# Kernel tuning notes

Measured on AMD Instinct MI355X. Metric: run time of the kernel, lower is better.

The kernel has to match this reference:

```python
import jax, jax.numpy as jnp
import numpy as np

N_NODES = 50000
N_EDGES = 800000
D_FEAT = 64


def setup_inputs() -> dict:
    key = jax.random.key(0)
    k_x, k_e, k_w = jax.random.split(key, 3)
    x = jax.random.normal(k_x, (N_NODES, D_FEAT), dtype=jnp.float32)
    edge_index = jax.random.randint(k_e, (2, N_EDGES), 0, N_NODES, dtype=jnp.int64)
    # message MLP params (phi_Theta): single linear + ReLU
    W = jax.random.normal(k_w, (D_FEAT, D_FEAT), dtype=jnp.float32) / np.sqrt(D_FEAT)
    b = jnp.zeros((D_FEAT,), dtype=jnp.float32)
    return {"x": x, "edge_index": edge_index, "W": W, "b": b}


def reference(x, edge_index, W, b):
    # flow = source_to_target: messages flow from edge_index[0] (j) to edge_index[1] (i)
    src = edge_index[0]  # j: source nodes (gather)
    dst = edge_index[1]  # i: target nodes (scatter index)
    n_nodes = x.shape[0]
    # __collect__: index_select gather of source node features -> x_j [E, D]
    x_j = x[src]
    # message: per-edge MLP  phi(x_j) = relu(x_j W + b)
    msg = jax.nn.relu(jnp.einsum('ed,df->ef', x_j, W) + b)
    # aggregate: scatter-add into target nodes (aggr='add', dim_size = size_i)
    out = jax.ops.segment_sum(msg, dst, num_segments=n_nodes)
    # update: identity
    return out
```

## Files before the change

kernel.cpp:

```cpp
#include <hip/hip_runtime.h>
#include <hip/hip_bf16.h>

#define D 64
#define CAP 32
#define OVF_CAP 16384
#define NSHARD 8

__device__ __forceinline__ float bf2f(unsigned short u) {
    return __uint_as_float((unsigned int)u << 16);
}
__device__ __forceinline__ unsigned short f2bf(float f) {
    unsigned int u = __float_as_uint(f);
    unsigned int r = (u + 0x7fffu + ((u >> 16) & 1u)) >> 16;
    return (unsigned short)r;
}

__global__ __launch_bounds__(256) void node_mlp_kernel(
    const float* __restrict__ x, const float* __restrict__ W,
    const float* __restrict__ b, unsigned short* __restrict__ m,
    int* __restrict__ cnt, int* __restrict__ ovf_cnt, int n_nodes) {
    for (int i = blockIdx.x * blockDim.x + threadIdx.x; i < n_nodes;
         i += gridDim.x * blockDim.x) cnt[i] = 0;
    if (blockIdx.x == 0 && threadIdx.x == 0) *ovf_cnt = 0;

    const int lane = threadIdx.x & 63;
    float w[D];
    #pragma unroll
    for (int k = 0; k < D; ++k) w[k] = W[k * D + lane];
    const float bias = b[lane];

    const int wave = (blockIdx.x * blockDim.x + threadIdx.x) >> 6;
    const int nwaves = (gridDim.x * blockDim.x) >> 6;

    for (int row = wave; row < n_nodes; row += nwaves) {
        const float4* xr = (const float4*)(x + (size_t)row * D);
        float acc = bias;
        #pragma unroll
        for (int kk = 0; kk < D / 4; ++kk) {
            float4 xv = xr[kk];
            acc = fmaf(xv.x, w[4 * kk + 0], acc);
            acc = fmaf(xv.y, w[4 * kk + 1], acc);
            acc = fmaf(xv.z, w[4 * kk + 2], acc);
            acc = fmaf(xv.w, w[4 * kk + 3], acc);
        }
        m[(size_t)row * D + lane] = f2bf(fmaxf(acc, 0.0f));
    }
}

__global__ __launch_bounds__(256) void append_kernel(
    const int* __restrict__ src, const int* __restrict__ dst,
    int* __restrict__ cnt, unsigned short* __restrict__ slots,
    int* __restrict__ ovf_cnt, unsigned int* __restrict__ ovf,
    int n_edges, int blocks_per_shard) {
    const int shard = blockIdx.x & (NSHARD - 1);
    const int p = blockIdx.x >> 3;
    const int chunk = (n_edges + blocks_per_shard - 1) / blocks_per_shard;
    const int beg = p * chunk;
    const int end = min(beg + chunk, n_edges);

    for (int e = beg + (int)threadIdx.x; e < end; e += 256) {
        int d = dst[e];
        if ((d & (NSHARD - 1)) != shard) continue;
        int s = src[e];
        int pos = atomicAdd(&cnt[d], 1);
        if (pos < CAP) {
            slots[(size_t)d * CAP + pos] = (unsigned short)s;
        } else {
            int op = atomicAdd(ovf_cnt, 1);
            if (op < OVF_CAP)
                ovf[op] = ((unsigned int)d << 16) | (unsigned int)s;
        }
    }
}

__global__ __launch_bounds__(256) void gather_kernel(
    const unsigned short* __restrict__ slots, const int* __restrict__ cnt,
    const unsigned short* __restrict__ m,
    const int* __restrict__ ovf_cnt, const unsigned int* __restrict__ ovf,
    float* __restrict__ out, int n_nodes) {
    const int grp = blockIdx.x >> 3;
    const int xcd = blockIdx.x & 7;
    int node = grp * 32 + ((threadIdx.x >> 6) << 3) + xcd;
    if (node >= n_nodes) return;
    node = __builtin_amdgcn_readfirstlane(node);

    const int lane = threadIdx.x & 63;

    const int c = cnt[node];
    const int cc = min(c, CAP);
    const unsigned int* __restrict__ row =
        (const unsigned int*)(slots + (size_t)node * CAP);

    float acc = 0.0f;
    int k = 0;
    for (; k + 16 <= cc; k += 16) {
        unsigned int p[8];
        #pragma unroll
        for (int i = 0; i < 8; ++i) p[i] = row[(k >> 1) + i];
        float v[16];
        #pragma unroll
        for (int i = 0; i < 8; ++i) {
            const unsigned short* ba = m + (size_t)(p[i] & 0xFFFFu) * D;
            const unsigned short* bb = m + (size_t)(p[i] >> 16) * D;
            v[2 * i + 0] = bf2f(ba[lane]);
            v[2 * i + 1] = bf2f(bb[lane]);
        }
        float t0 = ((v[0] + v[1]) + (v[2] + v[3])) + ((v[4] + v[5]) + (v[6] + v[7]));
        float t1 = ((v[8] + v[9]) + (v[10] + v[11])) + ((v[12] + v[13]) + (v[14] + v[15]));
        acc += t0 + t1;
    }
    for (; k + 4 <= cc; k += 4) {
        unsigned int p0 = row[(k >> 1) + 0];
        unsigned int p1 = row[(k >> 1) + 1];
        const unsigned short* b0 = m + (size_t)(p0 & 0xFFFFu) * D;
        const unsigned short* b1 = m + (size_t)(p0 >> 16) * D;
        const unsigned short* b2 = m + (size_t)(p1 & 0xFFFFu) * D;
        const unsigned short* b3 = m + (size_t)(p1 >> 16) * D;
        float v0 = bf2f(b0[lane]);
        float v1 = bf2f(b1[lane]);
        float v2 = bf2f(b2[lane]);
        float v3 = bf2f(b3[lane]);
        acc += (v0 + v1) + (v2 + v3);
    }
    for (; k < cc; ++k) {
        unsigned int p = row[k >> 1];
        unsigned int s = (k & 1) ? (p >> 16) : (p & 0xFFFFu);
        acc += bf2f(m[(size_t)s * D + lane]);
    }
    if (c > CAP) {
        int oc = min(*ovf_cnt, OVF_CAP);
        for (int i = 0; i < oc; ++i) {
            unsigned int e = ovf[i];
            if ((int)(e >> 16) == node)
                acc += bf2f(m[(size_t)(e & 0xFFFFu) * D + lane]);
        }
    }
    out[(size_t)node * D + lane] = acc;
}

__global__ __launch_bounds__(256) void edge_scatter_kernel(
    const int* __restrict__ src, const int* __restrict__ dst,
    const unsigned short* __restrict__ m, float* __restrict__ out, int n_edges) {
    long long t = (long long)blockIdx.x * blockDim.x + threadIdx.x;
    int e = (int)(t >> 4);
    if (e >= n_edges) return;
    int c = (int)(t & 15) << 2;
    int s = src[e];
    int d = dst[e];
    const ushort4 v = *(const ushort4*)(m + (size_t)s * D + c);
    float* o = out + (size_t)d * D + c;
    atomicAdd(o + 0, bf2f(v.x));
    atomicAdd(o + 1, bf2f(v.y));
    atomicAdd(o + 2, bf2f(v.z));
    atomicAdd(o + 3, bf2f(v.w));
}

static inline size_t align_up(size_t v, size_t a) { return (v + a - 1) & ~(a - 1); }

extern "C" void kernel_launch(void* const* d_in, const int* in_sizes, int n_in,
                              void* d_out, int out_size, void* d_ws, size_t ws_size,
                              hipStream_t stream) {
    const float* x = (const float*)d_in[0];
    const int* edge_index = (const int*)d_in[1];
    const float* W = (const float*)d_in[2];
    const float* b = (const float*)d_in[3];
    float* out = (float*)d_out;

    const int n_nodes = in_sizes[0] / D;
    const int n_edges = in_sizes[1] / 2;
    const int* src = edge_index;
    const int* dst = edge_index + n_edges;

    size_t off = 0;
    unsigned short* m = (unsigned short*)((char*)d_ws + off);
    off = align_up(off + (size_t)n_nodes * D * sizeof(unsigned short), 256);
    int* cnt = (int*)((char*)d_ws + off);
    off = align_up(off + (size_t)n_nodes * sizeof(int), 256);
    unsigned short* slots = (unsigned short*)((char*)d_ws + off);
    off = align_up(off + (size_t)n_nodes * CAP * sizeof(unsigned short), 256);
    int* ovf_cnt = (int*)((char*)d_ws + off);
    off = align_up(off + sizeof(int), 256);
    unsigned int* ovf = (unsigned int*)((char*)d_ws + off);
    off = align_up(off + (size_t)OVF_CAP * sizeof(unsigned int), 256);
    const size_t needed = off;

    node_mlp_kernel<<<512, 256, 0, stream>>>(x, W, b, m, cnt, ovf_cnt, n_nodes);

    if (ws_size >= needed && n_nodes <= 65536) {
        const int blocks_per_shard = 320;
        append_kernel<<<blocks_per_shard * NSHARD, 256, 0, stream>>>(
            src, dst, cnt, slots, ovf_cnt, ovf, n_edges, blocks_per_shard);
        const int ngroups = (n_nodes + 31) / 32;
        gather_kernel<<<ngroups * 8, 256, 0, stream>>>(
            slots, cnt, m, ovf_cnt, ovf, out, n_nodes);
    } else {
        hipMemsetAsync(d_out, 0, (size_t)out_size * sizeof(float), stream);
        long long total_threads = (long long)n_edges * 16;
        int scat_blocks = (int)((total_threads + 255) / 256);
        edge_scatter_kernel<<<scat_blocks, 256, 0, stream>>>(src, dst, m, out, n_edges);
    }
}
```

Measured before the change: 156.1 us.

## Fuse MLP, append and gather into one persistent kernel with grid barriers

Replaces the three separate launches (node MLP, slot append, gather) with a single persistent kernel of 1024 blocks. The phases are separated by a hand-rolled atomic grid barrier, and each phase is grid-strided. The aim is to remove kernel launch gaps and tail effects between stages. In exchange it adds a memset for the barrier counters and spin-wait cost at each barrier. It also risks deadlock if all 1024 blocks are not co-resident, because this is not a cooperative launch.

```diff
diff --git a/kernel.cpp b/kernel.cpp
--- a/kernel.cpp
+++ b/kernel.cpp
@@ -5,6 +5,7 @@
 #define CAP 32
 #define OVF_CAP 16384
 #define NSHARD 8
+#define COOP_BLOCKS 1024
 
 __device__ __forceinline__ float bf2f(unsigned short u) {
     return __uint_as_float((unsigned int)u << 16);
@@ -15,23 +16,153 @@
     return (unsigned short)r;
 }
 
+__device__ __forceinline__ void grid_sync_manual(unsigned int* bar, unsigned int nb) {
+    __syncthreads();
+    if (threadIdx.x == 0) {
+        __threadfence();
+        atomicAdd(bar, 1u);
+        while (__hip_atomic_load(bar, __ATOMIC_RELAXED,
+                                 __HIP_MEMORY_SCOPE_AGENT) < nb) {
+            __builtin_amdgcn_s_sleep(8);
+        }
+        __threadfence();
+    }
+    __syncthreads();
+}
+
+__global__ __launch_bounds__(256, 4) void fused_all_kernel(
+    const float* __restrict__ x, const float* __restrict__ W,
+    const float* __restrict__ b, const int* __restrict__ src,
+    const int* __restrict__ dst, unsigned short* __restrict__ m,
+    int* __restrict__ cnt, unsigned short* __restrict__ slots,
+    int* __restrict__ ovf_cnt, unsigned int* __restrict__ ovf,
+    unsigned int* __restrict__ bar, float* __restrict__ out,
+    int n_nodes, int n_edges) {
+    const int tid = threadIdx.x;
+    const int nb = gridDim.x;
+    const int lane = tid & 63;
+
+    for (int i = blockIdx.x * 256 + tid; i < n_nodes; i += nb * 256) cnt[i] = 0;
+    if (blockIdx.x == 0 && tid == 0) *ovf_cnt = 0;
+    {
+        float w[D];
+        #pragma unroll
+        for (int k = 0; k < D; ++k) w[k] = W[k * D + lane];
+        const float bias = b[lane];
+        const int wave = (blockIdx.x * 256 + tid) >> 6;
+        const int nwaves = (nb * 256) >> 6;
+        for (int row = wave; row < n_nodes; row += nwaves) {
+            const float4* xr = (const float4*)(x + (size_t)row * D);
+            float acc = bias;
+            #pragma unroll
+            for (int kk = 0; kk < D / 4; ++kk) {
+                float4 xv = xr[kk];
+                acc = fmaf(xv.x, w[4 * kk + 0], acc);
+                acc = fmaf(xv.y, w[4 * kk + 1], acc);
+                acc = fmaf(xv.z, w[4 * kk + 2], acc);
+                acc = fmaf(xv.w, w[4 * kk + 3], acc);
+            }
+            m[(size_t)row * D + lane] = f2bf(fmaxf(acc, 0.0f));
+        }
+    }
+    grid_sync_manual(&bar[0], nb);
+
+    {
+        const int shard = blockIdx.x & (NSHARD - 1);
+        const int p = blockIdx.x >> 3;
+        const int bps = nb >> 3;
+        const int chunk = (n_edges + bps - 1) / bps;
+        const int beg = p * chunk;
+        const int end = min(beg + chunk, n_edges);
+        for (int e = beg + tid; e < end; e += 256) {
+            int d = dst[e];
+            if ((d & (NSHARD - 1)) != shard) continue;
+            int s = src[e];
+            int pos = atomicAdd(&cnt[d], 1);
+            if (pos < CAP) {
+                slots[(size_t)d * CAP + pos] = (unsigned short)s;
+            } else {
+                int op = atomicAdd(ovf_cnt, 1);
+                if (op < OVF_CAP)
+                    ovf[op] = ((unsigned int)d << 16) | (unsigned int)s;
+            }
+        }
+    }
+    grid_sync_manual(&bar[1], nb);
+
+    {
+        const int xcd = blockIdx.x & 7;
+        const int ngroups = (n_nodes + 31) / 32;
+        const int gstride = nb >> 3;
+        for (int g = blockIdx.x >> 3; g < ngroups; g += gstride) {
+            int node = g * 32 + ((tid >> 6) << 3) + xcd;
+            if (node >= n_nodes) continue;
+            node = __builtin_amdgcn_readfirstlane(node);
+
+            const int c = cnt[node];
+            const int cc = min(c, CAP);
+            const unsigned int* __restrict__ row =
+                (const unsigned int*)(slots + (size_t)node * CAP);
+
+            float acc = 0.0f;
+            int k = 0;
+            for (; k + 16 <= cc; k += 16) {
+                unsigned int p[8];
+                #pragma unroll
+                for (int i = 0; i < 8; ++i) p[i] = row[(k >> 1) + i];
+                float v[16];
+                #pragma unroll
+                for (int i = 0; i < 8; ++i) {
+                    const unsigned short* ba = m + (size_t)(p[i] & 0xFFFFu) * D;
+                    const unsigned short* bb = m + (size_t)(p[i] >> 16) * D;
+                    v[2 * i + 0] = bf2f(ba[lane]);
+                    v[2 * i + 1] = bf2f(bb[lane]);
+                }
+                float t0 = ((v[0] + v[1]) + (v[2] + v[3])) + ((v[4] + v[5]) + (v[6] + v[7]));
+                float t1 = ((v[8] + v[9]) + (v[10] + v[11])) + ((v[12] + v[13]) + (v[14] + v[15]));
+                acc += t0 + t1;
+            }
+            for (; k + 4 <= cc; k += 4) {
+                unsigned int p0 = row[(k >> 1) + 0];
+                unsigned int p1 = row[(k >> 1) + 1];
+                const unsigned short* b0 = m + (size_t)(p0 & 0xFFFFu) * D;
+                const unsigned short* b1 = m + (size_t)(p0 >> 16) * D;
+                const unsigned short* b2 = m + (size_t)(p1 & 0xFFFFu) * D;
+                const unsigned short* b3 = m + (size_t)(p1 >> 16) * D;
+                float v0 = bf2f(b0[lane]);
+                float v1 = bf2f(b1[lane]);
+                float v2 = bf2f(b2[lane]);
+                float v3 = bf2f(b3[lane]);
+                acc += (v0 + v1) + (v2 + v3);
+            }
+            for (; k < cc; ++k) {
+                unsigned int p = row[k >> 1];
+                unsigned int s = (k & 1) ? (p >> 16) : (p & 0xFFFFu);
+                acc += bf2f(m[(size_t)s * D + lane]);
+            }
+            if (c > CAP) {
+                int oc = min(*(volatile int*)ovf_cnt, OVF_CAP);
+                for (int i = 0; i < oc; ++i) {
+                    unsigned int e = ovf[i];
+                    if ((int)(e >> 16) == node)
+                        acc += bf2f(m[(size_t)(e & 0xFFFFu) * D + lane]);
+                }
+            }
+            out[(size_t)node * D + lane] = acc;
+        }
+    }
+}
+
 __global__ __launch_bounds__(256) void node_mlp_kernel(
     const float* __restrict__ x, const float* __restrict__ W,
-    const float* __restrict__ b, unsigned short* __restrict__ m,
-    int* __restrict__ cnt, int* __restrict__ ovf_cnt, int n_nodes) {
-    for (int i = blockIdx.x * blockDim.x + threadIdx.x; i < n_nodes;
-         i += gridDim.x * blockDim.x) cnt[i] = 0;
-    if (blockIdx.x == 0 && threadIdx.x == 0) *ovf_cnt = 0;
-
+    const float* __restrict__ b, unsigned short* __restrict__ m, int n_nodes) {
     const int lane = threadIdx.x & 63;
     float w[D];
     #pragma unroll
     for (int k = 0; k < D; ++k) w[k] = W[k * D + lane];
     const float bias = b[lane];
-
     const int wave = (blockIdx.x * blockDim.x + threadIdx.x) >> 6;
     const int nwaves = (gridDim.x * blockDim.x) >> 6;
-
     for (int row = wave; row < n_nodes; row += nwaves) {
         const float4* xr = (const float4*)(x + (size_t)row * D);
         float acc = bias;
@@ -45,97 +176,6 @@
         }
         m[(size_t)row * D + lane] = f2bf(fmaxf(acc, 0.0f));
     }
-}
-
-__global__ __launch_bounds__(256) void append_kernel(
-    const int* __restrict__ src, const int* __restrict__ dst,
-    int* __restrict__ cnt, unsigned short* __restrict__ slots,
-    int* __restrict__ ovf_cnt, unsigned int* __restrict__ ovf,
-    int n_edges, int blocks_per_shard) {
-    const int shard = blockIdx.x & (NSHARD - 1);
-    const int p = blockIdx.x >> 3;
-    const int chunk = (n_edges + blocks_per_shard - 1) / blocks_per_shard;
-    const int beg = p * chunk;
-    const int end = min(beg + chunk, n_edges);
-
-    for (int e = beg + (int)threadIdx.x; e < end; e += 256) {
-        int d = dst[e];
-        if ((d & (NSHARD - 1)) != shard) continue;
-        int s = src[e];
-        int pos = atomicAdd(&cnt[d], 1);
-        if (pos < CAP) {
-            slots[(size_t)d * CAP + pos] = (unsigned short)s;
-        } else {
-            int op = atomicAdd(ovf_cnt, 1);
-            if (op < OVF_CAP)
-                ovf[op] = ((unsigned int)d << 16) | (unsigned int)s;
-        }
-    }
-}
-
-__global__ __launch_bounds__(256) void gather_kernel(
-    const unsigned short* __restrict__ slots, const int* __restrict__ cnt,
-    const unsigned short* __restrict__ m,
-    const int* __restrict__ ovf_cnt, const unsigned int* __restrict__ ovf,
-    float* __restrict__ out, int n_nodes) {
-    const int grp = blockIdx.x >> 3;
-    const int xcd = blockIdx.x & 7;
-    int node = grp * 32 + ((threadIdx.x >> 6) << 3) + xcd;
-    if (node >= n_nodes) return;
-    node = __builtin_amdgcn_readfirstlane(node);
-
-    const int lane = threadIdx.x & 63;
-
-    const int c = cnt[node];
-    const int cc = min(c, CAP);
-    const unsigned int* __restrict__ row =
-        (const unsigned int*)(slots + (size_t)node * CAP);
-
-    float acc = 0.0f;
-    int k = 0;
-    for (; k + 16 <= cc; k += 16) {
-        unsigned int p[8];
-        #pragma unroll
-        for (int i = 0; i < 8; ++i) p[i] = row[(k >> 1) + i];
-        float v[16];
-        #pragma unroll
-        for (int i = 0; i < 8; ++i) {
-            const unsigned short* ba = m + (size_t)(p[i] & 0xFFFFu) * D;
-            const unsigned short* bb = m + (size_t)(p[i] >> 16) * D;
-            v[2 * i + 0] = bf2f(ba[lane]);
-            v[2 * i + 1] = bf2f(bb[lane]);
-        }
-        float t0 = ((v[0] + v[1]) + (v[2] + v[3])) + ((v[4] + v[5]) + (v[6] + v[7]));
-        float t1 = ((v[8] + v[9]) + (v[10] + v[11])) + ((v[12] + v[13]) + (v[14] + v[15]));
-        acc += t0 + t1;
-    }
-    for (; k + 4 <= cc; k += 4) {
-        unsigned int p0 = row[(k >> 1) + 0];
-        unsigned int p1 = row[(k >> 1) + 1];
-        const unsigned short* b0 = m + (size_t)(p0 & 0xFFFFu) * D;
-        const unsigned short* b1 = m + (size_t)(p0 >> 16) * D;
-        const unsigned short* b2 = m + (size_t)(p1 & 0xFFFFu) * D;
-        const unsigned short* b3 = m + (size_t)(p1 >> 16) * D;
-        float v0 = bf2f(b0[lane]);
-        float v1 = bf2f(b1[lane]);
-        float v2 = bf2f(b2[lane]);
-        float v3 = bf2f(b3[lane]);
-        acc += (v0 + v1) + (v2 + v3);
-    }
-    for (; k < cc; ++k) {
-        unsigned int p = row[k >> 1];
-        unsigned int s = (k & 1) ? (p >> 16) : (p & 0xFFFFu);
-        acc += bf2f(m[(size_t)s * D + lane]);
-    }
-    if (c > CAP) {
-        int oc = min(*ovf_cnt, OVF_CAP);
-        for (int i = 0; i < oc; ++i) {
-            unsigned int e = ovf[i];
-            if ((int)(e >> 16) == node)
-                acc += bf2f(m[(size_t)(e & 0xFFFFu) * D + lane]);
-        }
-    }
-    out[(size_t)node * D + lane] = acc;
 }
 
 __global__ __launch_bounds__(256) void edge_scatter_kernel(
@@ -182,18 +222,17 @@
     off = align_up(off + sizeof(int), 256);
     unsigned int* ovf = (unsigned int*)((char*)d_ws + off);
     off = align_up(off + (size_t)OVF_CAP * sizeof(unsigned int), 256);
+    unsigned int* bar = (unsigned int*)((char*)d_ws + off);
+    off = align_up(off + 2 * sizeof(unsigned int), 256);
     const size_t needed = off;
 
-    node_mlp_kernel<<<512, 256, 0, stream>>>(x, W, b, m, cnt, ovf_cnt, n_nodes);
-
     if (ws_size >= needed && n_nodes <= 65536) {
-        const int blocks_per_shard = 320;
-        append_kernel<<<blocks_per_shard * NSHARD, 256, 0, stream>>>(
-            src, dst, cnt, slots, ovf_cnt, ovf, n_edges, blocks_per_shard);
-        const int ngroups = (n_nodes + 31) / 32;
-        gather_kernel<<<ngroups * 8, 256, 0, stream>>>(
-            slots, cnt, m, ovf_cnt, ovf, out, n_nodes);
+        hipMemsetAsync(bar, 0, 2 * sizeof(unsigned int), stream);
+        fused_all_kernel<<<COOP_BLOCKS, 256, 0, stream>>>(
+            x, W, b, src, dst, m, cnt, slots, ovf_cnt, ovf, bar, out,
+            n_nodes, n_edges);
     } else {
+        node_mlp_kernel<<<512, 256, 0, stream>>>(x, W, b, m, n_nodes);
         hipMemsetAsync(d_out, 0, (size_t)out_size * sizeof(float), stream);
         long long total_threads = (long long)n_edges * 16;
         int scat_blocks = (int)((total_threads + 255) / 256);
```

New measurement: 543.1 us. 248% more time.
